# Kernel tuning notes

Hardware: AMD Instinct MI355X
Metric: run time of the kernel (lower is better)

## Reference

```python
import jax, jax.numpy as jnp
import numpy as np

B, K, V, D, L = 16, 4, 32000, 512, 32   # batch, beam, vocab, d_model, max_decode_length
ALPHA, EOS = 0.6, 2
NEG_INF = 1.0e7   # matches inf('float32') in the torch source


def setup_inputs() -> dict:
    key = jax.random.key(0)
    k1, k2, k3, k4 = jax.random.split(key, 4)
    return {
        "initial_ids": jax.random.randint(k1, (B,), 0, V, dtype=jnp.int32),
        "init_cache_h": jax.random.normal(k2, (B, D), jnp.float32),
        "embed": jax.random.normal(k3, (V, D), jnp.float32) * 0.02,
        "proj": jax.random.normal(k4, (D, V), jnp.float32) * 0.02,
    }


def _beam_search(initial_ids, init_cache_h, embed, proj):
    # initial state (padded seq of length L+1; token 0 slot holds initial ids)
    alive_seq = jnp.zeros((B, K, L + 1), jnp.int32).at[:, :, 0].set(initial_ids[:, None])
    alive_lp = jnp.tile(jnp.array([[0.0] + [-NEG_INF] * (K - 1)], jnp.float32), (B, 1))
    cache_h = jnp.broadcast_to(init_cache_h[:, None, :], (B, K, D))
    fin_seq = jnp.zeros((B, K, L + 1), jnp.int32)
    fin_sc = jnp.full((B, K), -NEG_INF, jnp.float32)
    fin_fl = jnp.zeros((B, K), bool)

    def step(state, i):
        alive_seq, alive_lp, cache_h, fin_seq, fin_sc, fin_fl = state
        # symbols_to_logits_fn: tanh-RNN LM on the last emitted token
        last = alive_seq[:, :, i]                       # [B,K] traced index -> dynamic slice
        h = jnp.tanh(cache_h + embed[last])             # [B,K,D]
        logits = jnp.einsum('bkd,dv->bkv', h, proj)     # [B,K,V]
        # log-prob combine over flattened beam*vocab, keep 2K candidates
        lp = jax.nn.log_softmax(logits, axis=-1) + alive_lp[:, :, None]
        topk_lp, topk_idx = jax.lax.top_k(lp.reshape(B, K * V), 2 * K)
        beam_idx = topk_idx // V                        # [B,2K]
        ids = topk_idx % V
        # gather beams (seq + cache) and append new token at position i+1
        topk_seq = jnp.take_along_axis(alive_seq, beam_idx[:, :, None], axis=1)
        topk_seq = topk_seq.at[:, :, i + 1].set(ids)
        new_h = jnp.take_along_axis(h, beam_idx[:, :, None], axis=1)
        new_fl = ids == EOS                             # [B,2K]
        # new alive: penalize finished, keep top K
        alive_sc = topk_lp + new_fl.astype(jnp.float32) * -NEG_INF
        n_alive_lp, top_i = jax.lax.top_k(alive_sc, K)
        n_alive_seq = jnp.take_along_axis(topk_seq, top_i[:, :, None], axis=1)
        n_cache = jnp.take_along_axis(new_h, top_i[:, :, None], axis=1)
        # new finished: length-normalized scores, merge with previous finished
        ln = ((5.0 + (i + 1).astype(jnp.float32)) / 6.0) ** ALPHA
        new_scores = topk_lp / ln + (1.0 - new_fl.astype(jnp.float32)) * -NEG_INF
        comb_seq = jnp.concatenate([fin_seq, topk_seq], axis=1)   # [B,3K,L+1]
        comb_sc = jnp.concatenate([fin_sc, new_scores], axis=1)
        comb_fl = jnp.concatenate([fin_fl, new_fl], axis=1)
        n_fin_sc, top_fi = jax.lax.top_k(comb_sc, K)
        n_fin_seq = jnp.take_along_axis(comb_seq, top_fi[:, :, None], axis=1)
        n_fin_fl = jnp.take_along_axis(comb_fl, top_fi, axis=1)
        return (n_alive_seq, n_alive_lp, n_cache, n_fin_seq, n_fin_sc, n_fin_fl), None

    state0 = (alive_seq, alive_lp, cache_h, fin_seq, fin_sc, fin_fl)
    (alive_seq, alive_lp, _, fin_seq, fin_sc, fin_fl), _ = jax.lax.scan(
        step, state0, jnp.arange(L))
    # _process_finished_state: fall back to alive beams if nothing finished
    any_fin = jnp.any(fin_fl, axis=1)
    seq = jnp.where(any_fin[:, None, None], fin_seq.astype(jnp.float32),
                    alive_seq.astype(jnp.float32))
    sc = jnp.where(any_fin[:, None], fin_sc, alive_lp)
    return seq, sc


def reference(initial_ids, init_cache_h, embed, proj):
    return _beam_search(initial_ids, init_cache_h, embed, proj)
```

## Files before the change

### kernel.cpp

```cpp
#include <hip/hip_runtime.h>
#include <math.h>

#define BB 16
#define KK 4
#define VV 32000
#define DD 512
#define LL 32
#define EOS_ID 2
#define NEGINF 1.0e7f
#define ALPHA_C 0.6f
#define NROW (BB * KK)
#define NCHUNK 8
#define CHSZ (VV / NCHUNK)
#define SPLIT_S 2048.0f

typedef _Float16 f16x8 __attribute__((ext_vector_type(8)));
typedef float f32x4 __attribute__((ext_vector_type(4)));

#define GLOAD_LDS16(gp, lp) \
    __builtin_amdgcn_global_load_lds( \
        (const __attribute__((address_space(1))) void*)(gp), \
        (__attribute__((address_space(3))) void*)(lp), 16, 0, 0)

__device__ inline void pack_h(int r, int d, float v,
                              _Float16* __restrict__ hfrag_hi,
                              _Float16* __restrict__ hfrag_lo) {
    _Float16 hi = (_Float16)v;
    _Float16 lo = (_Float16)((v - (float)hi) * SPLIT_S);
    int rg = r >> 4;
    int ks = d >> 5;
    int lane = (r & 15) + 16 * ((d >> 3) & 3);
    int e = d & 7;
    int off = (((rg * 16 + ks) * 64) + lane) * 8 + e;
    hfrag_hi[off] = hi;
    hfrag_lo[off] = lo;
}

__global__ void k_init(const int* __restrict__ initial_ids,
                       int* alive_seq, float* alive_lp,
                       int* fin_seq, float* fin_sc, int* fin_fl) {
    int tid = blockIdx.x * blockDim.x + threadIdx.x;
    int nthreads = gridDim.x * blockDim.x;
    const int SEQ = NROW * (LL + 1);
    for (int idx = tid; idx < SEQ; idx += nthreads) {
        int pos = idx % (LL + 1);
        int b = (idx / (LL + 1)) / KK;
        alive_seq[idx] = (pos == 0) ? initial_ids[b] : 0;
        fin_seq[idx] = 0;
    }
    for (int idx = tid; idx < NROW; idx += nthreads) {
        int k = idx % KK;
        alive_lp[idx] = (k == 0) ? 0.0f : -NEGINF;
        fin_sc[idx] = -NEGINF;
        fin_fl[idx] = 0;
    }
}

__global__ __launch_bounds__(256) void k_bconv(const float* __restrict__ proj,
                                               _Float16* __restrict__ bfrag_hi,
                                               _Float16* __restrict__ bfrag_lo) {
    int ct = blockIdx.x;
    int t = threadIdx.x;
    int w = t >> 6, l = t & 63;
    int col = ct * 16 + (l & 15);
    int kg = l >> 4;
    for (int ks = w; ks < 16; ks += 4) {
        int k0 = ks * 32 + kg * 8;
        f16x8 hi, lo;
        #pragma unroll
        for (int j = 0; j < 8; j++) {
            float v = proj[(size_t)(k0 + j) * VV + col];
            _Float16 h = (_Float16)v;
            hi[j] = h;
            lo[j] = (_Float16)((v - (float)h) * SPLIT_S);
        }
        size_t off = (size_t)(ct * 16 + ks) * 64 + l;
        reinterpret_cast<f16x8*>(bfrag_hi)[off] = hi;
        reinterpret_cast<f16x8*>(bfrag_lo)[off] = lo;
    }
}

__global__ void k_hinit(const int* __restrict__ initial_ids,
                        const float* __restrict__ init_h,
                        const float* __restrict__ embed,
                        float* __restrict__ h_buf,
                        _Float16* __restrict__ hfrag_hi,
                        _Float16* __restrict__ hfrag_lo) {
    int row = blockIdx.x;
    int b = row >> 2;
    int t = threadIdx.x;
    int tok = initial_ids[b];
    for (int d = t; d < DD; d += 256) {
        float v = tanhf(init_h[b * DD + d] + embed[(size_t)tok * DD + d]);
        h_buf[row * DD + d] = v;
        pack_h(row, d, v, hfrag_hi, hfrag_lo);
    }
}

__global__ __launch_bounds__(256) void k_logits(
        const _Float16* __restrict__ bfrag_hi,
        const _Float16* __restrict__ bfrag_lo,
        const _Float16* __restrict__ hfrag_hi,
        const _Float16* __restrict__ hfrag_lo,
        float* __restrict__ logits) {
    int t = threadIdx.x;
    int w = t >> 6, l = t & 63;
    int ct0 = blockIdx.x * 4;
    int c0 = ct0 * 16;
    int colr = l & 15;
    int kg = l >> 4;
    int lq = l * 8;

    __shared__ _Float16 Bs[4][4][2][512];

    f16x8 ah[16], al[16];
    #pragma unroll
    for (int ks = 0; ks < 16; ks++) {
        ah[ks] = *reinterpret_cast<const f16x8*>(hfrag_hi + ((w * 16 + ks) * 64 + l) * 8);
        al[ks] = *reinterpret_cast<const f16x8*>(hfrag_lo + ((w * 16 + ks) * 64 + l) * 8);
    }
    __builtin_amdgcn_sched_barrier(0);

    f32x4 acc1[4], acc2[4];
    #pragma unroll
    for (int c2 = 0; c2 < 4; c2++) {
        acc1[c2] = (f32x4){0.f, 0.f, 0.f, 0.f};
        acc2[c2] = (f32x4){0.f, 0.f, 0.f, 0.f};
    }

    auto stage = [&](int s) {
        const _Float16* gh = bfrag_hi + (((size_t)(ct0 + w) * 16 + s) * 64 + l) * 8;
        const _Float16* gl = bfrag_lo + (((size_t)(ct0 + w) * 16 + s) * 64 + l) * 8;
        GLOAD_LDS16(gh, &Bs[s & 3][w][0][0]);
        GLOAD_LDS16(gl, &Bs[s & 3][w][1][0]);
    };

    stage(0); stage(1); stage(2); stage(3);

#define ITER(ks, NWAIT)                                                         \
    {                                                                           \
        asm volatile("s_waitcnt vmcnt(" #NWAIT ")" ::: "memory");               \
        __builtin_amdgcn_s_barrier();                                           \
        f16x8 bq[4][2];                                                         \
        _Pragma("unroll")                                                       \
        for (int c2 = 0; c2 < 4; c2++) {                                        \
            bq[c2][0] = *reinterpret_cast<const f16x8*>(&Bs[(ks) & 3][c2][0][lq]); \
            bq[c2][1] = *reinterpret_cast<const f16x8*>(&Bs[(ks) & 3][c2][1][lq]); \
        }                                                                       \
        asm volatile("s_waitcnt lgkmcnt(0)" ::: "memory");                      \
        __builtin_amdgcn_s_barrier();                                           \
        if ((ks) + 4 < 16) stage((ks) + 4);                                     \
        _Pragma("unroll")                                                       \
        for (int c2 = 0; c2 < 4; c2++) {                                        \
            acc1[c2] = __builtin_amdgcn_mfma_f32_16x16x32_f16(ah[(ks)], bq[c2][0], acc1[c2], 0, 0, 0); \
            acc2[c2] = __builtin_amdgcn_mfma_f32_16x16x32_f16(ah[(ks)], bq[c2][1], acc2[c2], 0, 0, 0); \
            acc2[c2] = __builtin_amdgcn_mfma_f32_16x16x32_f16(al[(ks)], bq[c2][0], acc2[c2], 0, 0, 0); \
        }                                                                       \
    }

    ITER(0, 6)  ITER(1, 6)  ITER(2, 6)  ITER(3, 6)
    ITER(4, 6)  ITER(5, 6)  ITER(6, 6)  ITER(7, 6)
    ITER(8, 6)  ITER(9, 6)  ITER(10, 6) ITER(11, 6)
    ITER(12, 6) ITER(13, 4) ITER(14, 2) ITER(15, 0)
#undef ITER

    #pragma unroll
    for (int c2 = 0; c2 < 4; c2++) {
        #pragma unroll
        for (int j = 0; j < 4; j++) {
            int row = w * 16 + kg * 4 + j;
            logits[(size_t)row * VV + c0 + c2 * 16 + colr] =
                acc1[c2][j] + acc2[c2][j] * (1.0f / SPLIT_S);
        }
    }
}

__global__ __launch_bounds__(256) void k_rowpart(
        const float* __restrict__ logits,
        float* __restrict__ ptop_val, int* __restrict__ ptop_idx,
        float* __restrict__ pmax, float* __restrict__ psum) {
    int chunk = blockIdx.x;
    int row = blockIdx.y;
    int t = threadIdx.x;
    int cbeg = chunk * CHSZ;
    const float4* lg4 = reinterpret_cast<const float4*>(logits + (size_t)row * VV + cbeg);

    float lv[8]; int li[8];
    #pragma unroll
    for (int j = 0; j < 8; j++) { lv[j] = -INFINITY; li[j] = 0x7fffffff; }
    float m = -INFINITY, s = 0.0f;
    for (int i = t; i < CHSZ / 4; i += 256) {
        float4 v4 = lg4[i];
        #pragma unroll
        for (int j2 = 0; j2 < 4; j2++) {
            float v = (j2 == 0) ? v4.x : (j2 == 1) ? v4.y : (j2 == 2) ? v4.z : v4.w;
            if (v > m) { s = s * expf(m - v) + 1.0f; m = v; }
            else       { s += expf(v - m); }
            if (v > lv[7]) {
                int c = cbeg + i * 4 + j2;
                int j = 7;
                while (j > 0 && v > lv[j - 1]) { lv[j] = lv[j - 1]; li[j] = li[j - 1]; j--; }
                lv[j] = v; li[j] = c;
            }
        }
    }
    __shared__ float sval[256][8];
    __shared__ int   sidx[256][8];
    __shared__ float sm[256], ss[256];
    #pragma unroll
    for (int j = 0; j < 8; j++) { sval[t][j] = lv[j]; sidx[t][j] = li[j]; }
    sm[t] = m; ss[t] = s;
    __syncthreads();
    for (int st = 128; st > 0; st >>= 1) {
        if (t < st) {
            float rv[8]; int ri[8];
            int pa = 0, pb = 0;
            #pragma unroll
            for (int j = 0; j < 8; j++) {
                bool aok = pa < 8, bok = pb < 8;
                float va = sval[t][aok ? pa : 7],     vb = sval[t + st][bok ? pb : 7];
                int   ia = sidx[t][aok ? pa : 7],     ib = sidx[t + st][bok ? pb : 7];
                bool takeA = !bok || (aok && ((va > vb) || (va == vb && ia <= ib)));
                if (takeA) { rv[j] = va; ri[j] = ia; pa++; }
                else       { rv[j] = vb; ri[j] = ib; pb++; }
            }
            #pragma unroll
            for (int j = 0; j < 8; j++) { sval[t][j] = rv[j]; sidx[t][j] = ri[j]; }
            float ma = sm[t], mb = sm[t + st];
            float M = fmaxf(ma, mb);
            ss[t] = ss[t] * expf(ma - M) + ss[t + st] * expf(mb - M);
            sm[t] = M;
        }
        __syncthreads();
    }
    if (t == 0) {
        #pragma unroll
        for (int j = 0; j < 8; j++) {
            ptop_val[(row * NCHUNK + chunk) * 8 + j] = sval[0][j];
            ptop_idx[(row * NCHUNK + chunk) * 8 + j] = sidx[0][j];
        }
        pmax[row * NCHUNK + chunk] = sm[0];
        psum[row * NCHUNK + chunk] = ss[0];
    }
}

__global__ __launch_bounds__(256) void k_update(
        const float* __restrict__ embed,
        float* h_buf, int* alive_seq, float* alive_lp,
        int* fin_seq, float* fin_sc, int* fin_fl,
        const float* __restrict__ ptop_val, const int* __restrict__ ptop_idx,
        const float* __restrict__ pmax, const float* __restrict__ psum,
        _Float16* __restrict__ hfrag_hi, _Float16* __restrict__ hfrag_lo,
        int step) {
    int b = blockIdx.x;
    int t = threadIdx.x;
    __shared__ float h_old[KK][DD];
    __shared__ int old_aseq[KK][LL + 1], old_fseq[KK][LL + 1];
    __shared__ float lse_s[KK], alp_s[KK];
    __shared__ float clp[256]; __shared__ int cidx[256];
    __shared__ float c_lp[8];  __shared__ int c_beam[8], c_id[8], c_fl[8];
    __shared__ float asc_s[8], comb_s[12]; __shared__ int combfl_s[12];
    __shared__ int sel_alive[KK], sel_fin[KK];
    __shared__ float n_alp[KK], n_fsc[KK]; __shared__ int n_ffl[KK];

    for (int idx = t; idx < KK * (LL + 1); idx += 256) {
        old_aseq[idx / (LL + 1)][idx % (LL + 1)] = alive_seq[b * KK * (LL + 1) + idx];
        old_fseq[idx / (LL + 1)][idx % (LL + 1)] = fin_seq[b * KK * (LL + 1) + idx];
    }
    for (int idx = t; idx < KK * DD; idx += 256)
        h_old[idx >> 9][idx & (DD - 1)] = h_buf[b * KK * DD + idx];
    if (t < KK) {
        int r = b * KK + t;
        float m = -INFINITY;
        #pragma unroll
        for (int c2 = 0; c2 < NCHUNK; c2++) m = fmaxf(m, pmax[r * NCHUNK + c2]);
        float s = 0.0f;
        #pragma unroll
        for (int c2 = 0; c2 < NCHUNK; c2++)
            s += psum[r * NCHUNK + c2] * expf(pmax[r * NCHUNK + c2] - m);
        lse_s[t] = m + logf(s);
        alp_s[t] = alive_lp[r];
    }
    __syncthreads();

    {
        int row = t >> 6;
        int src = ((b * KK + row) * NCHUNK + ((t >> 3) & 7)) * 8 + (t & 7);
        clp[t] = ptop_val[src] - lse_s[row] + alp_s[row];
        cidx[t] = ptop_idx[src];
    }
    __syncthreads();
    {
        int row = t >> 6;
        float mylp = clp[t];
        int mykey = row * VV + cidx[t];
        int cnt = 0;
        for (int j = 0; j < 256; j++) {
            float lj = clp[j];
            int kj = (j >> 6) * VV + cidx[j];
            cnt += (lj > mylp) || (lj == mylp && kj < mykey);
        }
        if (cnt < 8) {
            c_lp[cnt] = mylp; c_beam[cnt] = row; c_id[cnt] = cidx[t];
            c_fl[cnt] = (cidx[t] == EOS_ID) ? 1 : 0;
        }
    }
    __syncthreads();
    if (t < 8) asc_s[t] = c_lp[t] + (c_fl[t] ? -NEGINF : 0.0f);
    if (t >= 64 && t < 76) {
        int j2 = t - 64;
        if (j2 < 4) { comb_s[j2] = fin_sc[b * KK + j2]; combfl_s[j2] = fin_fl[b * KK + j2]; }
        else {
            int cc = j2 - 4;
            float ln = powf((6.0f + (float)step) / 6.0f, ALPHA_C);
            comb_s[j2] = c_lp[cc] / ln + (c_fl[cc] ? 0.0f : -NEGINF);
            combfl_s[j2] = c_fl[cc];
        }
    }
    __syncthreads();
    if (t < 8) {
        float a = asc_s[t];
        int cnt = 0;
        #pragma unroll
        for (int j = 0; j < 8; j++) cnt += (asc_s[j] > a) || (asc_s[j] == a && j < t);
        if (cnt < KK) { sel_alive[cnt] = t; n_alp[cnt] = a; }
    }
    if (t >= 64 && t < 76) {
        int j2 = t - 64;
        float cval = comb_s[j2];
        int cnt = 0;
        #pragma unroll
        for (int j = 0; j < 12; j++) cnt += (comb_s[j] > cval) || (comb_s[j] == cval && j < j2);
        if (cnt < KK) { sel_fin[cnt] = j2; n_fsc[cnt] = cval; n_ffl[cnt] = combfl_s[j2]; }
    }
    __syncthreads();

    for (int idx = t; idx < KK * (LL + 1); idx += 256) {
        int j = idx / (LL + 1), p = idx % (LL + 1);
        int cand = sel_alive[j], bm = c_beam[cand];
        alive_seq[b * KK * (LL + 1) + idx] = (p == step + 1) ? c_id[cand] : old_aseq[bm][p];
        int src = sel_fin[j];
        int fval;
        if (src < 4) fval = old_fseq[src][p];
        else {
            int c2 = src - 4, bm2 = c_beam[c2];
            fval = (p == step + 1) ? c_id[c2] : old_aseq[bm2][p];
        }
        fin_seq[b * KK * (LL + 1) + idx] = fval;
    }
    for (int idx = t; idx < KK * DD; idx += 256) {
        int j = idx >> 9, d = idx & (DD - 1);
        int cand = sel_alive[j], bm = c_beam[cand], tok = c_id[cand];
        float v = tanhf(h_old[bm][d] + embed[(size_t)tok * DD + d]);
        int r = b * KK + j;
        h_buf[(size_t)r * DD + d] = v;
        pack_h(r, d, v, hfrag_hi, hfrag_lo);
    }
    if (t < KK) {
        alive_lp[b * KK + t] = n_alp[t];
        fin_sc[b * KK + t] = n_fsc[t];
        fin_fl[b * KK + t] = n_ffl[t];
    }
}

__global__ void k_final(const int* __restrict__ alive_seq, const float* __restrict__ alive_lp,
                        const int* __restrict__ fin_seq, const float* __restrict__ fin_sc,
                        const int* __restrict__ fin_fl, float* __restrict__ out) {
    int b = blockIdx.x;
    int t = threadIdx.x;
    __shared__ int anyf;
    if (t == 0)
        anyf = fin_fl[b * KK] | fin_fl[b * KK + 1] | fin_fl[b * KK + 2] | fin_fl[b * KK + 3];
    __syncthreads();
    for (int idx = t; idx < KK * (LL + 1); idx += blockDim.x) {
        int src = anyf ? fin_seq[b * KK * (LL + 1) + idx] : alive_seq[b * KK * (LL + 1) + idx];
        out[b * KK * (LL + 1) + idx] = (float)src;
    }
    if (t < KK)
        out[BB * KK * (LL + 1) + b * KK + t] = anyf ? fin_sc[b * KK + t] : alive_lp[b * KK + t];
}

extern "C" void kernel_launch(void* const* d_in, const int* in_sizes, int n_in,
                              void* d_out, int out_size, void* d_ws, size_t ws_size,
                              hipStream_t stream) {
    const int* initial_ids = (const int*)d_in[0];
    const float* init_h = (const float*)d_in[1];
    const float* embed = (const float*)d_in[2];
    const float* proj = (const float*)d_in[3];
    float* out = (float*)d_out;

    char* ws = (char*)d_ws;
    size_t off = 0;
    auto alloc = [&](size_t bytes) -> void* {
        off = (off + 255) & ~(size_t)255;
        void* p = ws + off;
        off += bytes;
        return p;
    };
    int* alive_seq    = (int*)alloc((size_t)NROW * (LL + 1) * 4);
    int* fin_seq      = (int*)alloc((size_t)NROW * (LL + 1) * 4);
    float* alive_lp   = (float*)alloc((size_t)NROW * 4);
    float* fin_sc     = (float*)alloc((size_t)NROW * 4);
    int* fin_fl       = (int*)alloc((size_t)NROW * 4);
    float* h_buf      = (float*)alloc((size_t)NROW * DD * 4);
    float* logits     = (float*)alloc((size_t)NROW * VV * 4);
    float* ptop_val   = (float*)alloc((size_t)NROW * NCHUNK * 8 * 4);
    int* ptop_idx     = (int*)alloc((size_t)NROW * NCHUNK * 8 * 4);
    float* pmax       = (float*)alloc((size_t)NROW * NCHUNK * 4);
    float* psum       = (float*)alloc((size_t)NROW * NCHUNK * 4);
    _Float16* hfrag_hi = (_Float16*)alloc((size_t)NROW * DD * 2);
    _Float16* hfrag_lo = (_Float16*)alloc((size_t)NROW * DD * 2);
    _Float16* bfrag_hi = (_Float16*)alloc((size_t)VV * DD * 2);
    _Float16* bfrag_lo = (_Float16*)alloc((size_t)VV * DD * 2);

    k_init<<<16, 256, 0, stream>>>(initial_ids, alive_seq, alive_lp,
                                   fin_seq, fin_sc, fin_fl);
    k_bconv<<<2000, 256, 0, stream>>>(proj, bfrag_hi, bfrag_lo);
    k_hinit<<<NROW, 256, 0, stream>>>(initial_ids, init_h, embed, h_buf,
                                      hfrag_hi, hfrag_lo);
    for (int step = 0; step < LL; step++) {
        k_logits<<<500, 256, 0, stream>>>(bfrag_hi, bfrag_lo, hfrag_hi, hfrag_lo, logits);
        k_rowpart<<<dim3(NCHUNK, NROW), 256, 0, stream>>>(logits, ptop_val, ptop_idx,
                                                          pmax, psum);
        k_update<<<BB, 256, 0, stream>>>(embed, h_buf, alive_seq, alive_lp,
                                         fin_seq, fin_sc, fin_fl,
                                         ptop_val, ptop_idx, pmax, psum,
                                         hfrag_hi, hfrag_lo, step);
    }
    k_final<<<BB, 64, 0, stream>>>(alive_seq, alive_lp, fin_seq, fin_sc, fin_fl, out);
}
```

Before: 1.676 ms.

## Fuse per-tile top-8 and softmax stats into logits GEMM, add merge kernel

Each logits block now keeps its 64x64 tile in LDS, computes a per-row top-8 and online max/sum there, and writes only those partials instead of the full logits matrix. A new per-row merge kernel reduces the 500 block partials to a row top-8 and log-sum-exp, and the update kernel only looks at 32 candidates per batch. The aim is to drop the 8 MB logits write and re-read each step. The load pipeline also goes from 4 to 6 LDS slots, and the insertion sort becomes branchless. In exchange there are more partial writes and a second reduction pass.

```diff
diff --git a/kernel.cpp b/kernel.cpp
--- a/kernel.cpp
+++ b/kernel.cpp
@@ -10,8 +10,8 @@
 #define NEGINF 1.0e7f
 #define ALPHA_C 0.6f
 #define NROW (BB * KK)
-#define NCHUNK 8
-#define CHSZ (VV / NCHUNK)
+#define NBLK 500
+#define NSLOT 6
 #define SPLIT_S 2048.0f
 
 typedef _Float16 f16x8 __attribute__((ext_vector_type(8)));
@@ -21,6 +21,19 @@
     __builtin_amdgcn_global_load_lds( \
         (const __attribute__((address_space(1))) void*)(gp), \
         (__attribute__((address_space(3))) void*)(lp), 16, 0, 0)
+
+#define INS8(v, idx, lv, li)                                          \
+    if ((v) > lv[7]) {                                                \
+        bool c_[8];                                                   \
+        _Pragma("unroll")                                             \
+        for (int j_ = 0; j_ < 8; j_++) c_[j_] = (v) > lv[j_];         \
+        _Pragma("unroll")                                             \
+        for (int j_ = 7; j_ >= 1; j_--) {                             \
+            lv[j_] = c_[j_] ? (c_[j_ - 1] ? lv[j_ - 1] : (v)) : lv[j_];   \
+            li[j_] = c_[j_] ? (c_[j_ - 1] ? li[j_ - 1] : (idx)) : li[j_]; \
+        }                                                             \
+        if (c_[0]) { lv[0] = (v); li[0] = (idx); }                    \
+    }
 
 __device__ inline void pack_h(int r, int d, float v,
                               _Float16* __restrict__ hfrag_hi,
@@ -102,7 +115,8 @@
         const _Float16* __restrict__ bfrag_lo,
         const _Float16* __restrict__ hfrag_hi,
         const _Float16* __restrict__ hfrag_lo,
-        float* __restrict__ logits) {
+        float* __restrict__ ptv, int* __restrict__ pti,
+        float* __restrict__ pm, float* __restrict__ ps) {
     int t = threadIdx.x;
     int w = t >> 6, l = t & 63;
     int ct0 = blockIdx.x * 4;
@@ -111,7 +125,7 @@
     int kg = l >> 4;
     int lq = l * 8;
 
-    __shared__ _Float16 Bs[4][4][2][512];
+    __shared__ _Float16 Bs[NSLOT][4][2][512];
 
     f16x8 ah[16], al[16];
     #pragma unroll
@@ -119,6 +133,7 @@
         ah[ks] = *reinterpret_cast<const f16x8*>(hfrag_hi + ((w * 16 + ks) * 64 + l) * 8);
         al[ks] = *reinterpret_cast<const f16x8*>(hfrag_lo + ((w * 16 + ks) * 64 + l) * 8);
     }
+    asm volatile("s_waitcnt vmcnt(0)" ::: "memory");
     __builtin_amdgcn_sched_barrier(0);
 
     f32x4 acc1[4], acc2[4];
@@ -129,13 +144,14 @@
     }
 
     auto stage = [&](int s) {
+        int slot = s % NSLOT;
         const _Float16* gh = bfrag_hi + (((size_t)(ct0 + w) * 16 + s) * 64 + l) * 8;
         const _Float16* gl = bfrag_lo + (((size_t)(ct0 + w) * 16 + s) * 64 + l) * 8;
-        GLOAD_LDS16(gh, &Bs[s & 3][w][0][0]);
-        GLOAD_LDS16(gl, &Bs[s & 3][w][1][0]);
+        GLOAD_LDS16(gh, &Bs[slot][w][0][0]);
+        GLOAD_LDS16(gl, &Bs[slot][w][1][0]);
     };
 
-    stage(0); stage(1); stage(2); stage(3);
+    stage(0); stage(1); stage(2); stage(3); stage(4); stage(5);
 
 #define ITER(ks, NWAIT)                                                         \
     {                                                                           \
@@ -144,12 +160,12 @@
         f16x8 bq[4][2];                                                         \
         _Pragma("unroll")                                                       \
         for (int c2 = 0; c2 < 4; c2++) {                                        \
-            bq[c2][0] = *reinterpret_cast<const f16x8*>(&Bs[(ks) & 3][c2][0][lq]); \
-            bq[c2][1] = *reinterpret_cast<const f16x8*>(&Bs[(ks) & 3][c2][1][lq]); \
+            bq[c2][0] = *reinterpret_cast<const f16x8*>(&Bs[(ks) % NSLOT][c2][0][lq]); \
+            bq[c2][1] = *reinterpret_cast<const f16x8*>(&Bs[(ks) % NSLOT][c2][1][lq]); \
         }                                                                       \
         asm volatile("s_waitcnt lgkmcnt(0)" ::: "memory");                      \
         __builtin_amdgcn_s_barrier();                                           \
-        if ((ks) + 4 < 16) stage((ks) + 4);                                     \
+        if ((ks) + NSLOT < 16) stage((ks) + NSLOT);                             \
         _Pragma("unroll")                                                       \
         for (int c2 = 0; c2 < 4; c2++) {                                        \
             acc1[c2] = __builtin_amdgcn_mfma_f32_16x16x32_f16(ah[(ks)], bq[c2][0], acc1[c2], 0, 0, 0); \
@@ -158,57 +174,111 @@
         }                                                                       \
     }
 
-    ITER(0, 6)  ITER(1, 6)  ITER(2, 6)  ITER(3, 6)
-    ITER(4, 6)  ITER(5, 6)  ITER(6, 6)  ITER(7, 6)
-    ITER(8, 6)  ITER(9, 6)  ITER(10, 6) ITER(11, 6)
-    ITER(12, 6) ITER(13, 4) ITER(14, 2) ITER(15, 0)
+    ITER(0, 10)  ITER(1, 10)  ITER(2, 10)  ITER(3, 10)
+    ITER(4, 10)  ITER(5, 10)  ITER(6, 10)  ITER(7, 10)
+    ITER(8, 10)  ITER(9, 10)  ITER(10, 10) ITER(11, 8)
+    ITER(12, 6)  ITER(13, 4)  ITER(14, 2)  ITER(15, 0)
 #undef ITER
 
-    #pragma unroll
-    for (int c2 = 0; c2 < 4; c2++) {
-        #pragma unroll
-        for (int j = 0; j < 4; j++) {
-            int row = w * 16 + kg * 4 + j;
-            logits[(size_t)row * VV + c0 + c2 * 16 + colr] =
+    char* pool = (char*)&Bs[0][0][0][0];
+    float* Cs  = (float*)pool;
+    float* sv  = (float*)(pool + 16640);
+    int*   si  = (int*)  (pool + 24832);
+    float* smx = (float*)(pool + 33024);
+    float* ssm = (float*)(pool + 34048);
+
+    #pragma unroll
+    for (int c2 = 0; c2 < 4; c2++)
+        #pragma unroll
+        for (int j = 0; j < 4; j++)
+            Cs[(w * 16 + kg * 4 + j) * 65 + c2 * 16 + colr] =
                 acc1[c2][j] + acc2[c2][j] * (1.0f / SPLIT_S);
-        }
-    }
-}
-
-__global__ __launch_bounds__(256) void k_rowpart(
-        const float* __restrict__ logits,
-        float* __restrict__ ptop_val, int* __restrict__ ptop_idx,
-        float* __restrict__ pmax, float* __restrict__ psum) {
-    int chunk = blockIdx.x;
-    int row = blockIdx.y;
-    int t = threadIdx.x;
-    int cbeg = chunk * CHSZ;
-    const float4* lg4 = reinterpret_cast<const float4*>(logits + (size_t)row * VV + cbeg);
-
+    __syncthreads();
+
+    int row = t >> 2, cg = t & 3;
     float lv[8]; int li[8];
     #pragma unroll
     for (int j = 0; j < 8; j++) { lv[j] = -INFINITY; li[j] = 0x7fffffff; }
     float m = -INFINITY, s = 0.0f;
-    for (int i = t; i < CHSZ / 4; i += 256) {
-        float4 v4 = lg4[i];
-        #pragma unroll
-        for (int j2 = 0; j2 < 4; j2++) {
-            float v = (j2 == 0) ? v4.x : (j2 == 1) ? v4.y : (j2 == 2) ? v4.z : v4.w;
-            if (v > m) { s = s * expf(m - v) + 1.0f; m = v; }
-            else       { s += expf(v - m); }
-            if (v > lv[7]) {
-                int c = cbeg + i * 4 + j2;
-                int j = 7;
-                while (j > 0 && v > lv[j - 1]) { lv[j] = lv[j - 1]; li[j] = li[j - 1]; j--; }
-                lv[j] = v; li[j] = c;
+    #pragma unroll
+    for (int cc = 0; cc < 16; cc++) {
+        float v = Cs[row * 65 + cg * 16 + cc];
+        int idx = c0 + cg * 16 + cc;
+        float M = fmaxf(m, v);
+        s = s * expf(m - M) + expf(v - M);
+        m = M;
+        INS8(v, idx, lv, li)
+    }
+    #pragma unroll
+    for (int j = 0; j < 8; j++) { sv[t * 8 + j] = lv[j]; si[t * 8 + j] = li[j]; }
+    smx[t] = m; ssm[t] = s;
+    __syncthreads();
+    for (int st = 2; st > 0; st >>= 1) {
+        if ((t & 3) < st) {
+            float rv[8]; int ri[8];
+            int pa = 0, pb = 0;
+            #pragma unroll
+            for (int j = 0; j < 8; j++) {
+                bool aok = pa < 8, bok = pb < 8;
+                float va = sv[t * 8 + (aok ? pa : 7)], vb = sv[(t + st) * 8 + (bok ? pb : 7)];
+                int   ia = si[t * 8 + (aok ? pa : 7)], ib = si[(t + st) * 8 + (bok ? pb : 7)];
+                bool takeA = !bok || (aok && ((va > vb) || (va == vb && ia <= ib)));
+                if (takeA) { rv[j] = va; ri[j] = ia; pa++; }
+                else       { rv[j] = vb; ri[j] = ib; pb++; }
             }
-        }
-    }
-    __shared__ float sval[256][8];
-    __shared__ int   sidx[256][8];
+            #pragma unroll
+            for (int j = 0; j < 8; j++) { sv[t * 8 + j] = rv[j]; si[t * 8 + j] = ri[j]; }
+            float ma = smx[t], mb = smx[t + st];
+            float M = fmaxf(ma, mb);
+            ssm[t] = ssm[t] * expf(ma - M) + ssm[t + st] * expf(mb - M);
+            smx[t] = M;
+        }
+        __syncthreads();
+    }
+    if ((t & 3) == 0) {
+        size_t base = ((size_t)row * NBLK + blockIdx.x) * 8;
+        #pragma unroll
+        for (int j = 0; j < 8; j++) { ptv[base + j] = sv[t * 8 + j]; pti[base + j] = si[t * 8 + j]; }
+        pm[(size_t)row * NBLK + blockIdx.x] = smx[t];
+        ps[(size_t)row * NBLK + blockIdx.x] = ssm[t];
+    }
+}
+
+__global__ __launch_bounds__(256) void k_merge(
+        const float* __restrict__ ptv, const int* __restrict__ pti,
+        const float* __restrict__ pm, const float* __restrict__ ps,
+        float* __restrict__ rowtop_val, int* __restrict__ rowtop_idx,
+        float* __restrict__ row_lse) {
+    int row = blockIdx.x, t = threadIdx.x;
+    __shared__ float sval[256][8]; __shared__ int sidx[256][8];
     __shared__ float sm[256], ss[256];
-    #pragma unroll
-    for (int j = 0; j < 8; j++) { sval[t][j] = lv[j]; sidx[t][j] = li[j]; }
+    const float* pv = ptv + (size_t)row * NBLK * 8;
+    const int*   pi = pti + (size_t)row * NBLK * 8;
+
+    #pragma unroll
+    for (int j = 0; j < 8; j++) { sval[t][j] = pv[t * 8 + j]; sidx[t][j] = pi[t * 8 + j]; }
+    float m = pm[(size_t)row * NBLK + t], s = ps[(size_t)row * NBLK + t];
+    if (t + 256 < NBLK) {
+        const float* bv = pv + (size_t)(t + 256) * 8;
+        const int*   bi = pi + (size_t)(t + 256) * 8;
+        float rv[8]; int ri[8];
+        int pa = 0, pb = 0;
+        #pragma unroll
+        for (int j = 0; j < 8; j++) {
+            bool aok = pa < 8, bok = pb < 8;
+            float va = sval[t][aok ? pa : 7], vb = bv[bok ? pb : 7];
+            int   ia = sidx[t][aok ? pa : 7], ib = bi[bok ? pb : 7];
+            bool takeA = !bok || (aok && ((va > vb) || (va == vb && ia <= ib)));
+            if (takeA) { rv[j] = va; ri[j] = ia; pa++; }
+            else       { rv[j] = vb; ri[j] = ib; pb++; }
+        }
+        #pragma unroll
+        for (int j = 0; j < 8; j++) { sval[t][j] = rv[j]; sidx[t][j] = ri[j]; }
+        float mb = pm[(size_t)row * NBLK + t + 256], sb = ps[(size_t)row * NBLK + t + 256];
+        float M = fmaxf(m, mb);
+        s = s * expf(m - M) + sb * expf(mb - M);
+        m = M;
+    }
     sm[t] = m; ss[t] = s;
     __syncthreads();
     for (int st = 128; st > 0; st >>= 1) {
@@ -218,8 +288,8 @@
             #pragma unroll
             for (int j = 0; j < 8; j++) {
                 bool aok = pa < 8, bok = pb < 8;
-                float va = sval[t][aok ? pa : 7],     vb = sval[t + st][bok ? pb : 7];
-                int   ia = sidx[t][aok ? pa : 7],     ib = sidx[t + st][bok ? pb : 7];
+                float va = sval[t][aok ? pa : 7], vb = sval[t + st][bok ? pb : 7];
+                int   ia = sidx[t][aok ? pa : 7], ib = sidx[t + st][bok ? pb : 7];
                 bool takeA = !bok || (aok && ((va > vb) || (va == vb && ia <= ib)));
                 if (takeA) { rv[j] = va; ri[j] = ia; pa++; }
                 else       { rv[j] = vb; ri[j] = ib; pb++; }
@@ -236,11 +306,10 @@
     if (t == 0) {
         #pragma unroll
         for (int j = 0; j < 8; j++) {
-            ptop_val[(row * NCHUNK + chunk) * 8 + j] = sval[0][j];
-            ptop_idx[(row * NCHUNK + chunk) * 8 + j] = sidx[0][j];
-        }
-        pmax[row * NCHUNK + chunk] = sm[0];
-        psum[row * NCHUNK + chunk] = ss[0];
+            rowtop_val[row * 8 + j] = sval[0][j];
+            rowtop_idx[row * 8 + j] = sidx[0][j];
+        }
+        row_lse[row] = sm[0] + logf(ss[0]);
     }
 }
 
@@ -248,8 +317,8 @@
         const float* __restrict__ embed,
         float* h_buf, int* alive_seq, float* alive_lp,
         int* fin_seq, float* fin_sc, int* fin_fl,
-        const float* __restrict__ ptop_val, const int* __restrict__ ptop_idx,
-        const float* __restrict__ pmax, const float* __restrict__ psum,
+        const float* __restrict__ rowtop_val, const int* __restrict__ rowtop_idx,
+        const float* __restrict__ row_lse,
         _Float16* __restrict__ hfrag_hi, _Float16* __restrict__ hfrag_lo,
         int step) {
     int b = blockIdx.x;
@@ -257,7 +326,7 @@
     __shared__ float h_old[KK][DD];
     __shared__ int old_aseq[KK][LL + 1], old_fseq[KK][LL + 1];
     __shared__ float lse_s[KK], alp_s[KK];
-    __shared__ float clp[256]; __shared__ int cidx[256];
+    __shared__ float clp[32]; __shared__ int cidx[32];
     __shared__ float c_lp[8];  __shared__ int c_beam[8], c_id[8], c_fl[8];
     __shared__ float asc_s[8], comb_s[12]; __shared__ int combfl_s[12];
     __shared__ int sel_alive[KK], sel_fin[KK];
@@ -271,34 +340,27 @@
         h_old[idx >> 9][idx & (DD - 1)] = h_buf[b * KK * DD + idx];
     if (t < KK) {
         int r = b * KK + t;
-        float m = -INFINITY;
-        #pragma unroll
-        for (int c2 = 0; c2 < NCHUNK; c2++) m = fmaxf(m, pmax[r * NCHUNK + c2]);
-        float s = 0.0f;
-        #pragma unroll
-        for (int c2 = 0; c2 < NCHUNK; c2++)
-            s += psum[r * NCHUNK + c2] * expf(pmax[r * NCHUNK + c2] - m);
-        lse_s[t] = m + logf(s);
+        lse_s[t] = row_lse[r];
         alp_s[t] = alive_lp[r];
     }
     __syncthreads();
 
-    {
-        int row = t >> 6;
-        int src = ((b * KK + row) * NCHUNK + ((t >> 3) & 7)) * 8 + (t & 7);
-        clp[t] = ptop_val[src] - lse_s[row] + alp_s[row];
-        cidx[t] = ptop_idx[src];
-    }
-    __syncthreads();
-    {
-        int row = t >> 6;
+    if (t < 32) {
+        int row = t >> 3;
+        int src = (b * KK + row) * 8 + (t & 7);
+        clp[t] = rowtop_val[src] - lse_s[row] + alp_s[row];
+        cidx[t] = rowtop_idx[src];
+    }
+    __syncthreads();
+    if (t < 32) {
+        int row = t >> 3;
         float mylp = clp[t];
         int mykey = row * VV + cidx[t];
         int cnt = 0;
-        for (int j = 0; j < 256; j++) {
-            float lj = clp[j];
-            int kj = (j >> 6) * VV + cidx[j];
-            cnt += (lj > mylp) || (lj == mylp && kj < mykey);
+        #pragma unroll
+        for (int j = 0; j < 32; j++) {
+            int kj = (j >> 3) * VV + cidx[j];
+            cnt += (clp[j] > mylp) || (clp[j] == mylp && kj < mykey);
         }
         if (cnt < 8) {
             c_lp[cnt] = mylp; c_beam[cnt] = row; c_id[cnt] = cidx[t];
@@ -403,11 +465,13 @@
     float* fin_sc     = (float*)alloc((size_t)NROW * 4);
     int* fin_fl       = (int*)alloc((size_t)NROW * 4);
     float* h_buf      = (float*)alloc((size_t)NROW * DD * 4);
-    float* logits     = (float*)alloc((size_t)NROW * VV * 4);
-    float* ptop_val   = (float*)alloc((size_t)NROW * NCHUNK * 8 * 4);
-    int* ptop_idx     = (int*)alloc((size_t)NROW * NCHUNK * 8 * 4);
-    float* pmax       = (float*)alloc((size_t)NROW * NCHUNK * 4);
-    float* psum       = (float*)alloc((size_t)NROW * NCHUNK * 4);
+    float* ptv        = (float*)alloc((size_t)NROW * NBLK * 8 * 4);
+    int* pti          = (int*)alloc((size_t)NROW * NBLK * 8 * 4);
+    float* pm         = (float*)alloc((size_t)NROW * NBLK * 4);
+    float* ps         = (float*)alloc((size_t)NROW * NBLK * 4);
+    float* rowtop_val = (float*)alloc((size_t)NROW * 8 * 4);
+    int* rowtop_idx   = (int*)alloc((size_t)NROW * 8 * 4);
+    float* row_lse    = (float*)alloc((size_t)NROW * 4);
     _Float16* hfrag_hi = (_Float16*)alloc((size_t)NROW * DD * 2);
     _Float16* hfrag_lo = (_Float16*)alloc((size_t)NROW * DD * 2);
     _Float16* bfrag_hi = (_Float16*)alloc((size_t)VV * DD * 2);
@@ -419,12 +483,13 @@
     k_hinit<<<NROW, 256, 0, stream>>>(initial_ids, init_h, embed, h_buf,
                                       hfrag_hi, hfrag_lo);
     for (int step = 0; step < LL; step++) {
-        k_logits<<<500, 256, 0, stream>>>(bfrag_hi, bfrag_lo, hfrag_hi, hfrag_lo, logits);
-        k_rowpart<<<dim3(NCHUNK, NROW), 256, 0, stream>>>(logits, ptop_val, ptop_idx,
-                                                          pmax, psum);
+        k_logits<<<NBLK, 256, 0, stream>>>(bfrag_hi, bfrag_lo, hfrag_hi, hfrag_lo,
+                                           ptv, pti, pm, ps);
+        k_merge<<<NROW, 256, 0, stream>>>(ptv, pti, pm, ps,
+                                          rowtop_val, rowtop_idx, row_lse);
         k_update<<<BB, 256, 0, stream>>>(embed, h_buf, alive_seq, alive_lp,
                                          fin_seq, fin_sc, fin_fl,
-                                         ptop_val, ptop_idx, pmax, psum,
+                                         rowtop_val, rowtop_idx, row_lse,
                                          hfrag_hi, hfrag_lo, step);
     }
     k_final<<<BB, 64, 0, stream>>>(alive_seq, alive_lp, fin_seq, fin_sc, fin_fl, out);
```

Result: faster. 1.470 ms, median of 2 (-12.3%).
